# Kernel optimization log

Measured on AMD Instinct MI355X. Metric: run time of the kernel, lower is better.

## Reference

```python
import jax, jax.numpy as jnp
import numpy as np

D_ATTN = 64


def setup_inputs() -> dict:
    key = jax.random.key(0)
    ks = jax.random.split(key, 10)
    B, N, D_MODEL = 8, 1024, 512
    s = 0.02
    return {
        "x": jax.random.normal(ks[0], (B, N, D_MODEL), jnp.float32),
        "top": jax.random.normal(ks[1], (B, N, N, 16), jnp.float32),
        "Wq": jax.random.normal(ks[2], (D_MODEL, D_ATTN), jnp.float32) * s,
        "bq": jnp.zeros((D_ATTN,), jnp.float32),
        "Wk": jax.random.normal(ks[3], (D_MODEL, D_ATTN), jnp.float32) * s,
        "bk": jnp.zeros((D_ATTN,), jnp.float32),
        "Wv": jax.random.normal(ks[4], (D_MODEL, D_ATTN), jnp.float32) * s,
        "bv": jnp.zeros((D_ATTN,), jnp.float32),
        "Wt": jax.random.normal(ks[5], (16, 1), jnp.float32) * s,
        "bt": jnp.zeros((1,), jnp.float32),
    }


def reference(x, top, Wq, bq, Wk, bk, Wv, bv, Wt, bt):
    # QKV projections: [B,N,d_model] -> [B,N,d_attn]
    Q = x @ Wq + bq
    K = x @ Wk + bk
    V = x @ Wv + bv
    scale = 1.0 / jnp.sqrt(jnp.asarray(D_ATTN, x.dtype))
    # [B,N,N] attention logits
    logits = jnp.einsum("bnd,bmd->bnm", Q, K) * scale
    # learned topological bias: Linear(16,1) on [B,N,N,16] -> [B,N,N]
    bias = jnp.einsum("bnmf,fo->bnmo", top, Wt)[..., 0] + bt[0]
    score = jax.nn.softmax(logits + bias, axis=-1)
    return jnp.einsum("bnm,bmd->bnd", score, V)
```

## Files before the change

### kernel.cpp

```cpp
#include <hip/hip_runtime.h>
#include <hip/hip_bf16.h>

typedef __attribute__((ext_vector_type(8))) short short8;
typedef __attribute__((ext_vector_type(4))) float f32x4;
typedef unsigned short ushort_t;
typedef unsigned int uint_t;

#define D_MODEL 512
#define D_ATTN  64
#define LROW 1032

__device__ __forceinline__ ushort_t f2bf(float f) {
    uint_t u = __float_as_uint(f);
    u += 0x7FFFu + ((u >> 16) & 1u);
    return (ushort_t)(u >> 16);
}
__device__ __forceinline__ float bf2f(ushort_t h) {
    return __uint_as_float((uint_t)h << 16);
}
__device__ __forceinline__ f32x4 ntload4(const f32x4* p) {
    return __builtin_nontemporal_load(p);
}

__global__ __launch_bounds__(256)
void qkv_all(const float* __restrict__ x,
             const float* __restrict__ Wq, const float* __restrict__ bq,
             const float* __restrict__ Wk, const float* __restrict__ bk,
             const float* __restrict__ Wv, const float* __restrict__ bv,
             ushort_t* __restrict__ Q, ushort_t* __restrict__ K,
             ushort_t* __restrict__ Vt)
{
    const int l = threadIdx.x & 63, w = threadIdx.x >> 6;
    const size_t bn0 = (size_t)blockIdx.x << 4;
    const int r0 = w << 2;
    const float* xb = x + (bn0 + r0) * D_MODEL;
    { uintptr_t u = (uintptr_t)xb; asm volatile("" : "+v"(u)); xb = (const float*)u; }

    float aq[4] = {0,0,0,0}, ak[4] = {0,0,0,0}, av[4] = {0,0,0,0};
#pragma unroll 2
    for (int k = 0; k < D_MODEL; k += 4) {
        float4 xr[4];
#pragma unroll
        for (int r = 0; r < 4; ++r) xr[r] = *(const float4*)(xb + r * D_MODEL + k);
        float wqv[4], wkv[4], wvv[4];
#pragma unroll
        for (int kk = 0; kk < 4; ++kk) {
            wqv[kk] = Wq[(k + kk) * D_ATTN + l];
            wkv[kk] = Wk[(k + kk) * D_ATTN + l];
            wvv[kk] = Wv[(k + kk) * D_ATTN + l];
        }
#pragma unroll
        for (int r = 0; r < 4; ++r) {
            const float xv[4] = {xr[r].x, xr[r].y, xr[r].z, xr[r].w};
#pragma unroll
            for (int kk = 0; kk < 4; ++kk) {
                aq[r] = fmaf(xv[kk], wqv[kk], aq[r]);
                ak[r] = fmaf(xv[kk], wkv[kk], ak[r]);
                av[r] = fmaf(xv[kk], wvv[kk], av[r]);
            }
        }
    }
    const float bqv = bq[l], bkv = bk[l], bvv = bv[l];
#pragma unroll
    for (int r = 0; r < 4; ++r) {
        Q[(bn0 + r0 + r) * D_ATTN + l] = f2bf((aq[r] + bqv) * 0.125f);
        K[(bn0 + r0 + r) * D_ATTN + l] = f2bf(ak[r] + bkv);
    }
    const int b = (int)(bn0 >> 10), n0loc = (int)(bn0 & 1023);
    uint2 pv;
    pv.x = (uint_t)f2bf(av[0] + bvv) | ((uint_t)f2bf(av[1] + bvv) << 16);
    pv.y = (uint_t)f2bf(av[2] + bvv) | ((uint_t)f2bf(av[3] + bvv) << 16);
    *(uint2*)(Vt + ((size_t)(b * 64 + l) << 10) + n0loc + r0) = pv;
}

__global__ __launch_bounds__(256, 4)
void topo_attn_f(const float* __restrict__ top, const float* __restrict__ Wt,
                 const ushort_t* __restrict__ Q, const ushort_t* __restrict__ K,
                 const ushort_t* __restrict__ Vt, float* __restrict__ out)
{
    __shared__ ushort_t sm[16 * LROW];
    __shared__ float redm[64], reds[64];
    const int tid = threadIdx.x;
    const int l = tid & 63, wv = tid >> 6;
    const int b   = blockIdx.x >> 6;
    const int bn0 = blockIdx.x << 4;

    {
        const f32x4* __restrict__ base = (const f32x4*)top + ((size_t)bn0 << 12);
        const float4 wq = *(const float4*)(Wt + ((l & 3) << 2));
        const int sel = l & 3;
        const f32x4* p0a = base + ((size_t)(wv << 2) << 12) + l;
        f32x4 c0 = ntload4(p0a), c1 = ntload4(p0a + 64),
              c2 = ntload4(p0a + 128), c3 = ntload4(p0a + 192);
        for (int it = 0; it < 64; ++it) {
            f32x4 n0, n1, n2, n3;
            if (it < 63) {
                int it1 = it + 1;
                const f32x4* q = base + ((size_t)((wv << 2) + (it1 >> 4)) << 12)
                                      + ((it1 & 15) << 8) + l;
                n0 = ntload4(q); n1 = ntload4(q + 64);
                n2 = ntload4(q + 128); n3 = ntload4(q + 192);
            }
            float p0 = c0[0] * wq.x; p0 = fmaf(c0[1], wq.y, p0); p0 = fmaf(c0[2], wq.z, p0); p0 = fmaf(c0[3], wq.w, p0);
            float p1 = c1[0] * wq.x; p1 = fmaf(c1[1], wq.y, p1); p1 = fmaf(c1[2], wq.z, p1); p1 = fmaf(c1[3], wq.w, p1);
            float p2 = c2[0] * wq.x; p2 = fmaf(c2[1], wq.y, p2); p2 = fmaf(c2[2], wq.z, p2); p2 = fmaf(c2[3], wq.w, p2);
            float p3 = c3[0] * wq.x; p3 = fmaf(c3[1], wq.y, p3); p3 = fmaf(c3[2], wq.z, p3); p3 = fmaf(c3[3], wq.w, p3);
            p0 += __shfl_xor(p0, 1); p0 += __shfl_xor(p0, 2);
            p1 += __shfl_xor(p1, 1); p1 += __shfl_xor(p1, 2);
            p2 += __shfl_xor(p2, 1); p2 += __shfl_xor(p2, 2);
            p3 += __shfl_xor(p3, 1); p3 += __shfl_xor(p3, 2);
            float pr = (sel == 0) ? p0 : (sel == 1) ? p1 : (sel == 2) ? p2 : p3;
            int rloc = (wv << 2) + (it >> 4);
            int m = ((it & 15) << 6) + (l >> 2) + (sel << 4);
            sm[rloc * LROW + m] = f2bf(pr);
            c0 = n0; c1 = n1; c2 = n2; c3 = n3;
        }
    }
    __syncthreads();

    const int lq = l & 15, lg4 = l >> 4;
    f32x4 lgt[16];
    {
        const short8 qb0 = *(const short8*)(Q + ((size_t)(bn0 + lq)) * 64 + 8 * lg4);
        const short8 qb1 = *(const short8*)(Q + ((size_t)(bn0 + lq)) * 64 + 32 + 8 * lg4);
        const ushort_t* __restrict__ Kb = K + ((size_t)b << 16);
#pragma unroll 4
        for (int t = 0; t < 16; ++t) {
            int m0 = (wv << 8) + (t << 4);
            short8 kb0 = *(const short8*)(Kb + (size_t)(m0 + lq) * 64 + 8 * lg4);
            short8 kb1 = *(const short8*)(Kb + (size_t)(m0 + lq) * 64 + 32 + 8 * lg4);
            f32x4 acc = {0.f, 0.f, 0.f, 0.f};
            acc = __builtin_amdgcn_mfma_f32_16x16x32_bf16(kb0, qb0, acc, 0, 0, 0);
            acc = __builtin_amdgcn_mfma_f32_16x16x32_bf16(kb1, qb1, acc, 0, 0, 0);
#pragma unroll
            for (int j = 0; j < 4; ++j)
                acc[j] += bf2f(sm[lq * LROW + m0 + 4 * lg4 + j]);
            lgt[t] = acc;
        }
    }

    {
        float mx = lgt[0][0];
#pragma unroll
        for (int t = 0; t < 16; ++t)
#pragma unroll
            for (int j = 0; j < 4; ++j) mx = fmaxf(mx, lgt[t][j]);
        mx = fmaxf(mx, __shfl_xor(mx, 16));
        mx = fmaxf(mx, __shfl_xor(mx, 32));
        if (l < 16) redm[l * 4 + wv] = mx;
        __syncthreads();
        float gmx = fmaxf(fmaxf(redm[lq * 4 + 0], redm[lq * 4 + 1]),
                          fmaxf(redm[lq * 4 + 2], redm[lq * 4 + 3]));
        float s = 0.f;
#pragma unroll
        for (int t = 0; t < 16; ++t)
#pragma unroll
            for (int j = 0; j < 4; ++j) {
                float e = __expf(lgt[t][j] - gmx);
                lgt[t][j] = e; s += e;
            }
        s += __shfl_xor(s, 16);
        s += __shfl_xor(s, 32);
        if (l < 16) reds[l * 4 + wv] = s;
        __syncthreads();
        float inv = 1.0f / (reds[lq * 4 + 0] + reds[lq * 4 + 1]
                          + reds[lq * 4 + 2] + reds[lq * 4 + 3]);
#pragma unroll
        for (int t = 0; t < 16; ++t) {
            int mbase = (wv << 8) + (t << 4) + 4 * lg4;
            uint_t w01 = (uint_t)f2bf(lgt[t][0] * inv) | ((uint_t)f2bf(lgt[t][1] * inv) << 16);
            uint_t w23 = (uint_t)f2bf(lgt[t][2] * inv) | ((uint_t)f2bf(lgt[t][3] * inv) << 16);
            *(uint_t*)(sm + lq * LROW + mbase)     = w01;
            *(uint_t*)(sm + lq * LROW + mbase + 2) = w23;
        }
    }
    __syncthreads();

    {
        f32x4 oe = {0,0,0,0}, oo = {0,0,0,0};
        const ushort_t* __restrict__ Vb = Vt + ((size_t)b << 16)
                                        + ((size_t)((wv << 4) + lq) << 10);
        const ushort_t* __restrict__ pb = sm + lq * LROW + 8 * lg4;
#pragma unroll 4
        for (int kk = 0; kk < 32; kk += 2) {
            short8 pa0 = *(const short8*)(pb + (kk << 5));
            short8 vb0 = *(const short8*)(Vb + (kk << 5) + 8 * lg4);
            oe = __builtin_amdgcn_mfma_f32_16x16x32_bf16(pa0, vb0, oe, 0, 0, 0);
            short8 pa1 = *(const short8*)(pb + (kk << 5) + 32);
            short8 vb1 = *(const short8*)(Vb + (kk << 5) + 32 + 8 * lg4);
            oo = __builtin_amdgcn_mfma_f32_16x16x32_bf16(pa1, vb1, oo, 0, 0, 0);
        }
#pragma unroll
        for (int j = 0; j < 4; ++j)
            out[((size_t)(bn0 + 4 * lg4 + j) << 6) + (wv << 4) + lq] = oe[j] + oo[j];
    }
}

extern "C" void kernel_launch(void* const* d_in, const int* in_sizes, int n_in,
                              void* d_out, int out_size, void* d_ws, size_t ws_size,
                              hipStream_t stream) {
    const float* x   = (const float*)d_in[0];
    const float* top = (const float*)d_in[1];
    const float* Wq  = (const float*)d_in[2];
    const float* bq  = (const float*)d_in[3];
    const float* Wk  = (const float*)d_in[4];
    const float* bk  = (const float*)d_in[5];
    const float* Wv  = (const float*)d_in[6];
    const float* bv  = (const float*)d_in[7];
    const float* Wt  = (const float*)d_in[8];
    float* out = (float*)d_out;

    ushort_t* Q  = (ushort_t*)d_ws;
    ushort_t* K  = Q + 8 * 1024 * 64;
    ushort_t* Vt = K + 8 * 1024 * 64;

    qkv_all<<<512, 256, 0, stream>>>(x, Wq, bq, Wk, bk, Wv, bv, Q, K, Vt);
    topo_attn_f<<<512, 256, 0, stream>>>(top, Wt, Q, K, Vt, out);
}
```

Before: 179.0 us.

## Stream topo bias through triple-buffered LDS via global_load_lds and widen QKV rows

The topological bias stage now loads `top` with asynchronous global-to-LDS loads into a three-stage shared buffer. Each iteration waits on the vector-memory counter and a barrier, instead of each lane prefetching four nontemporal vectors into registers. The QKV projection kernel handles 8 rows per wave instead of 4 and launches half as many blocks, so each weight load is reused across more rows. The new pipeline adds about 24KB of LDS and two barriers per chunk, which may lower occupancy. The launch-bounds occupancy hint is also removed.

```diff
diff --git a/kernel.cpp b/kernel.cpp
--- a/kernel.cpp
+++ b/kernel.cpp
@@ -18,9 +18,10 @@
 __device__ __forceinline__ float bf2f(ushort_t h) {
     return __uint_as_float((uint_t)h << 16);
 }
-__device__ __forceinline__ f32x4 ntload4(const f32x4* p) {
-    return __builtin_nontemporal_load(p);
-}
+
+#define GLOAD16(g, s) __builtin_amdgcn_global_load_lds(                         \
+    (const __attribute__((address_space(1))) unsigned int*)(g),                 \
+    (__attribute__((address_space(3))) unsigned int*)(s), 16, 0, 0)
 
 __global__ __launch_bounds__(256)
 void qkv_all(const float* __restrict__ x,
@@ -31,17 +32,19 @@
              ushort_t* __restrict__ Vt)
 {
     const int l = threadIdx.x & 63, w = threadIdx.x >> 6;
-    const size_t bn0 = (size_t)blockIdx.x << 4;
-    const int r0 = w << 2;
+    const size_t bn0 = (size_t)blockIdx.x << 5;
+    const int r0 = w << 3;
     const float* xb = x + (bn0 + r0) * D_MODEL;
     { uintptr_t u = (uintptr_t)xb; asm volatile("" : "+v"(u)); xb = (const float*)u; }
 
-    float aq[4] = {0,0,0,0}, ak[4] = {0,0,0,0}, av[4] = {0,0,0,0};
-#pragma unroll 2
+    float aq[8], ak[8], av[8];
+#pragma unroll
+    for (int r = 0; r < 8; ++r) { aq[r] = 0.f; ak[r] = 0.f; av[r] = 0.f; }
+
     for (int k = 0; k < D_MODEL; k += 4) {
-        float4 xr[4];
-#pragma unroll
-        for (int r = 0; r < 4; ++r) xr[r] = *(const float4*)(xb + r * D_MODEL + k);
+        float4 xr[8];
+#pragma unroll
+        for (int r = 0; r < 8; ++r) xr[r] = *(const float4*)(xb + r * D_MODEL + k);
         float wqv[4], wkv[4], wvv[4];
 #pragma unroll
         for (int kk = 0; kk < 4; ++kk) {
@@ -50,7 +53,7 @@
             wvv[kk] = Wv[(k + kk) * D_ATTN + l];
         }
 #pragma unroll
-        for (int r = 0; r < 4; ++r) {
+        for (int r = 0; r < 8; ++r) {
             const float xv[4] = {xr[r].x, xr[r].y, xr[r].z, xr[r].w};
 #pragma unroll
             for (int kk = 0; kk < 4; ++kk) {
@@ -62,58 +65,71 @@
     }
     const float bqv = bq[l], bkv = bk[l], bvv = bv[l];
 #pragma unroll
-    for (int r = 0; r < 4; ++r) {
+    for (int r = 0; r < 8; ++r) {
         Q[(bn0 + r0 + r) * D_ATTN + l] = f2bf((aq[r] + bqv) * 0.125f);
         K[(bn0 + r0 + r) * D_ATTN + l] = f2bf(ak[r] + bkv);
     }
     const int b = (int)(bn0 >> 10), n0loc = (int)(bn0 & 1023);
-    uint2 pv;
-    pv.x = (uint_t)f2bf(av[0] + bvv) | ((uint_t)f2bf(av[1] + bvv) << 16);
-    pv.y = (uint_t)f2bf(av[2] + bvv) | ((uint_t)f2bf(av[3] + bvv) << 16);
-    *(uint2*)(Vt + ((size_t)(b * 64 + l) << 10) + n0loc + r0) = pv;
-}
-
-__global__ __launch_bounds__(256, 4)
+    uint_t pk[4];
+#pragma unroll
+    for (int r = 0; r < 8; r += 2)
+        pk[r >> 1] = (uint_t)f2bf(av[r] + bvv) | ((uint_t)f2bf(av[r + 1] + bvv) << 16);
+    *(uint4*)(Vt + ((size_t)(b * 64 + l) << 10) + n0loc + r0) =
+        make_uint4(pk[0], pk[1], pk[2], pk[3]);
+}
+
+__global__ __launch_bounds__(256)
 void topo_attn_f(const float* __restrict__ top, const float* __restrict__ Wt,
                  const ushort_t* __restrict__ Q, const ushort_t* __restrict__ K,
                  const ushort_t* __restrict__ Vt, float* __restrict__ out)
 {
-    __shared__ ushort_t sm[16 * LROW];
+    __shared__ __align__(16) float stage[3 * 2048];
+    __shared__ __align__(16) ushort_t sm[16 * LROW];
     __shared__ float redm[64], reds[64];
     const int tid = threadIdx.x;
-    const int l = tid & 63, wv = tid >> 6;
+    const int l = tid & 63, w = tid >> 6;
     const int b   = blockIdx.x >> 6;
     const int bn0 = blockIdx.x << 4;
 
     {
-        const f32x4* __restrict__ base = (const f32x4*)top + ((size_t)bn0 << 12);
+        const float* __restrict__ topb = top + ((size_t)bn0 << 14);
         const float4 wq = *(const float4*)(Wt + ((l & 3) << 2));
-        const int sel = l & 3;
-        const f32x4* p0a = base + ((size_t)(wv << 2) << 12) + l;
-        f32x4 c0 = ntload4(p0a), c1 = ntload4(p0a + 64),
-              c2 = ntload4(p0a + 128), c3 = ntload4(p0a + 192);
-        for (int it = 0; it < 64; ++it) {
-            f32x4 n0, n1, n2, n3;
-            if (it < 63) {
-                int it1 = it + 1;
-                const f32x4* q = base + ((size_t)((wv << 2) + (it1 >> 4)) << 12)
-                                      + ((it1 & 15) << 8) + l;
-                n0 = ntload4(q); n1 = ntload4(q + 64);
-                n2 = ntload4(q + 128); n3 = ntload4(q + 192);
+        const int loff = (w << 9) + (l << 2);
+
+        {
+            const float* s0 = topb + loff;
+            GLOAD16(s0,       stage + (w << 9));
+            GLOAD16(s0 + 256, stage + (w << 9) + 256);
+            const float* s1 = topb + 2048 + loff;
+            GLOAD16(s1,       stage + 2048 + (w << 9));
+            GLOAD16(s1 + 256, stage + 2048 + (w << 9) + 256);
+        }
+        for (int c = 0; c < 128; ++c) {
+            int cc = (c + 2 > 127) ? 127 : (c + 2);
+            {
+                const float* s2 = topb + ((size_t)cc << 11) + loff;
+                float* d2 = stage + (cc % 3) * 2048 + (w << 9);
+                GLOAD16(s2,       d2);
+                GLOAD16(s2 + 256, d2 + 256);
             }
-            float p0 = c0[0] * wq.x; p0 = fmaf(c0[1], wq.y, p0); p0 = fmaf(c0[2], wq.z, p0); p0 = fmaf(c0[3], wq.w, p0);
-            float p1 = c1[0] * wq.x; p1 = fmaf(c1[1], wq.y, p1); p1 = fmaf(c1[2], wq.z, p1); p1 = fmaf(c1[3], wq.w, p1);
-            float p2 = c2[0] * wq.x; p2 = fmaf(c2[1], wq.y, p2); p2 = fmaf(c2[2], wq.z, p2); p2 = fmaf(c2[3], wq.w, p2);
-            float p3 = c3[0] * wq.x; p3 = fmaf(c3[1], wq.y, p3); p3 = fmaf(c3[2], wq.z, p3); p3 = fmaf(c3[3], wq.w, p3);
+            asm volatile("s_waitcnt vmcnt(4)" ::: "memory");
+            __builtin_amdgcn_s_barrier();
+            __builtin_amdgcn_sched_barrier(0);
+
+            const float* sb = stage + (c % 3) * 2048;
+            f32x4 u0 = *(const f32x4*)(sb + (((w << 7) + l) << 2));
+            f32x4 u1 = *(const f32x4*)(sb + (((w << 7) + 64 + l) << 2));
+            float p0 = u0[0] * wq.x; p0 = fmaf(u0[1], wq.y, p0);
+            p0 = fmaf(u0[2], wq.z, p0); p0 = fmaf(u0[3], wq.w, p0);
+            float p1 = u1[0] * wq.x; p1 = fmaf(u1[1], wq.y, p1);
+            p1 = fmaf(u1[2], wq.z, p1); p1 = fmaf(u1[3], wq.w, p1);
             p0 += __shfl_xor(p0, 1); p0 += __shfl_xor(p0, 2);
             p1 += __shfl_xor(p1, 1); p1 += __shfl_xor(p1, 2);
-            p2 += __shfl_xor(p2, 1); p2 += __shfl_xor(p2, 2);
-            p3 += __shfl_xor(p3, 1); p3 += __shfl_xor(p3, 2);
-            float pr = (sel == 0) ? p0 : (sel == 1) ? p1 : (sel == 2) ? p2 : p3;
-            int rloc = (wv << 2) + (it >> 4);
-            int m = ((it & 15) << 6) + (l >> 2) + (sel << 4);
-            sm[rloc * LROW + m] = f2bf(pr);
-            c0 = n0; c1 = n1; c2 = n2; c3 = n3;
+            int r  = c >> 3;
+            int mb = ((c & 7) << 7) + (w << 5) + (l >> 2);
+            if ((l & 3) == 0) sm[r * LROW + mb]      = f2bf(p0);
+            if ((l & 3) == 1) sm[r * LROW + mb + 16] = f2bf(p1);
+            __builtin_amdgcn_s_barrier();
         }
     }
     __syncthreads();
@@ -126,7 +142,7 @@
         const ushort_t* __restrict__ Kb = K + ((size_t)b << 16);
 #pragma unroll 4
         for (int t = 0; t < 16; ++t) {
-            int m0 = (wv << 8) + (t << 4);
+            int m0 = (w << 8) + (t << 4);
             short8 kb0 = *(const short8*)(Kb + (size_t)(m0 + lq) * 64 + 8 * lg4);
             short8 kb1 = *(const short8*)(Kb + (size_t)(m0 + lq) * 64 + 32 + 8 * lg4);
             f32x4 acc = {0.f, 0.f, 0.f, 0.f};
@@ -147,7 +163,7 @@
             for (int j = 0; j < 4; ++j) mx = fmaxf(mx, lgt[t][j]);
         mx = fmaxf(mx, __shfl_xor(mx, 16));
         mx = fmaxf(mx, __shfl_xor(mx, 32));
-        if (l < 16) redm[l * 4 + wv] = mx;
+        if (l < 16) redm[l * 4 + w] = mx;
         __syncthreads();
         float gmx = fmaxf(fmaxf(redm[lq * 4 + 0], redm[lq * 4 + 1]),
                           fmaxf(redm[lq * 4 + 2], redm[lq * 4 + 3]));
@@ -161,13 +177,13 @@
             }
         s += __shfl_xor(s, 16);
         s += __shfl_xor(s, 32);
-        if (l < 16) reds[l * 4 + wv] = s;
+        if (l < 16) reds[l * 4 + w] = s;
         __syncthreads();
         float inv = 1.0f / (reds[lq * 4 + 0] + reds[lq * 4 + 1]
                           + reds[lq * 4 + 2] + reds[lq * 4 + 3]);
 #pragma unroll
         for (int t = 0; t < 16; ++t) {
-            int mbase = (wv << 8) + (t << 4) + 4 * lg4;
+            int mbase = (w << 8) + (t << 4) + 4 * lg4;
             uint_t w01 = (uint_t)f2bf(lgt[t][0] * inv) | ((uint_t)f2bf(lgt[t][1] * inv) << 16);
             uint_t w23 = (uint_t)f2bf(lgt[t][2] * inv) | ((uint_t)f2bf(lgt[t][3] * inv) << 16);
             *(uint_t*)(sm + lq * LROW + mbase)     = w01;
@@ -179,7 +195,7 @@
     {
         f32x4 oe = {0,0,0,0}, oo = {0,0,0,0};
         const ushort_t* __restrict__ Vb = Vt + ((size_t)b << 16)
-                                        + ((size_t)((wv << 4) + lq) << 10);
+                                        + ((size_t)((w << 4) + lq) << 10);
         const ushort_t* __restrict__ pb = sm + lq * LROW + 8 * lg4;
 #pragma unroll 4
         for (int kk = 0; kk < 32; kk += 2) {
@@ -192,7 +208,7 @@
         }
 #pragma unroll
         for (int j = 0; j < 4; ++j)
-            out[((size_t)(bn0 + 4 * lg4 + j) << 6) + (wv << 4) + lq] = oe[j] + oo[j];
+            out[((size_t)(bn0 + 4 * lg4 + j) << 6) + (w << 4) + lq] = oe[j] + oo[j];
     }
 }
 
@@ -214,6 +230,6 @@
     ushort_t* K  = Q + 8 * 1024 * 64;
     ushort_t* Vt = K + 8 * 1024 * 64;
 
-    qkv_all<<<512, 256, 0, stream>>>(x, Wq, bq, Wk, bk, Wv, bv, Q, K, Vt);
+    qkv_all<<<256, 256, 0, stream>>>(x, Wq, bq, Wk, bk, Wv, bv, Q, K, Vt);
     topo_attn_f<<<512, 256, 0, stream>>>(top, Wt, Q, K, Vt, out);
 }
```

Result: slower. 267.9 us (+49.6%).
